# Kernel optimization log

Hardware: AMD Instinct MI355X
Metric: run time of the kernel (lower is better)

Reference implementation:

```python
import jax, jax.numpy as jnp
import numpy as np

TAU = 10.0          # tau_init
R_MAX = 8           # max(groupconvs)
GROUPCONVS = (4, 8)
PADS = (0, 8)       # (k - spat_red)//2 for k in (17, 33), spat_red = 33 - 2*8 = 17
NEG_SLOPE = 0.01    # LeakyReLU default


def lrelu(t):
    return jnp.where(t >= 0, t, NEG_SLOPE * t)


def rotate_kernel(w, theta):
    """Rotate square kernels w:[N,k,k] by theta, matching torch
    F.affine_grid + F.grid_sample (bilinear, zero padding, align_corners=False)."""
    N, k, _ = w.shape
    coords = (2.0 * jnp.arange(k) + 1.0) / k - 1.0  # normalized pixel centers
    gy, gx = jnp.meshgrid(coords, coords, indexing='ij')
    c, s = jnp.cos(theta), jnp.sin(theta)
    sx = c * gx - s * gy
    sy = s * gx + c * gy
    fx = ((sx + 1.0) * k - 1.0) / 2.0
    fy = ((sy + 1.0) * k - 1.0) / 2.0
    x0 = jnp.floor(fx).astype(jnp.int32)
    y0 = jnp.floor(fy).astype(jnp.int32)
    wf = w.reshape(N, k * k)

    def gather(yi, xi):
        valid = ((yi >= 0) & (yi < k) & (xi >= 0) & (xi < k)).astype(w.dtype)
        idx = jnp.clip(yi, 0, k - 1) * k + jnp.clip(xi, 0, k - 1)
        return wf[:, idx.reshape(-1)].reshape(N, k, k) * valid

    wx1 = fx - x0
    wy1 = fy - y0
    return (gather(y0, x0) * (1 - wy1) * (1 - wx1)
            + gather(y0, x0 + 1) * (1 - wy1) * wx1
            + gather(y0 + 1, x0) * wy1 * (1 - wx1)
            + gather(y0 + 1, x0 + 1) * wy1 * wx1)


def group_conv(x, w, b, pad):
    """GroupConv with input_rot_dim=1: x [B,1,H,W], w [O,1,1,k,k] -> [B,O,R_MAX,H',W']."""
    O, k = w.shape[0], w.shape[-1]
    w2 = w.reshape(O, k, k)
    angles = (2.0 * jnp.pi / R_MAX) * jnp.arange(R_MAX)
    tw = jax.vmap(lambda th: rotate_kernel(w2, th))(angles)   # [R,O,k,k]
    tw = jnp.transpose(tw, (1, 0, 2, 3)).reshape(O * R_MAX, 1, k, k)
    y = jax.lax.conv_general_dilated(x, tw, (1, 1), [(pad, pad), (pad, pad)],
                                     dimension_numbers=('NCHW', 'OIHW', 'NCHW'))
    B, _, H, W = y.shape
    return y.reshape(B, O, R_MAX, H, W) + b[None, :, None, None, None]


def conv1x1(h, w, b):
    # 1x1x1 Conv3d: h [B,C,R,H,W], w [O,C], b [O]
    return jnp.einsum('bcrhw,oc->borhw', h, w) + b[None, :, None, None, None]


def scatter_sum(outs, weights, axis):
    """slice_scatter-based alignment: embed smaller-rdim tensors into the
    largest one at stride max_dim//dim, weight, and sum."""
    max_out = outs[-1]
    md = max_out.shape[axis]
    total = max_out * weights[-1]
    for i, o in enumerate(outs[:-1]):
        step = md // o.shape[axis]
        idx = tuple(slice(None, None, step) if a == axis else slice(None)
                    for a in range(max_out.ndim))
        total = total + jnp.zeros_like(max_out).at[idx].set(o) * weights[i]
    return total


OFFSETS = np.array([0, np.pi / 4, np.pi / 2, 3 * np.pi / 4, np.pi,
                    -3 * np.pi / 4, -np.pi / 2, -np.pi / 4], dtype=np.float32)


def _forward(x, ksize_weight, rdim_weight, conv1_w0, conv1_b0, conv1_w1, conv1_b1,
             conv2_w, conv2_b, conva_w, conva_b, convz_w, convz_b,
             g_ksize, g_rdim, g_attn):
    # gumbel-softmax over kernel sizes (soft, tau=TAU)
    alphas = jax.nn.softmax((ksize_weight + g_ksize) / TAU)
    x_out = (alphas[0] * lrelu(group_conv(x, conv1_w0, conv1_b0, PADS[0]))
             + alphas[1] * lrelu(group_conv(x, conv1_w1, conv1_b1, PADS[1])))
    xs_out = [x_out[:, :, ::R_MAX // r] for r in GROUPCONVS]
    hs = [lrelu(conv1x1(xo, conv2_w[i], conv2_b[i])) for i, xo in enumerate(xs_out)]
    attns = [conv1x1(h, conva_w[i], conva_b[i])[:, 0] for i, h in enumerate(hs)]
    betas = jax.nn.softmax((rdim_weight + g_rdim) / TAU)
    attn = scatter_sum(attns, betas, axis=1)          # [B,R,H,W]
    offsets = jnp.asarray(OFFSETS)
    sigma = np.pi  # theta_prior; Normal(0, sigma) log-prob at offsets
    p_r = (-0.5 * (offsets / sigma) ** 2 - np.float32(np.log(sigma))
           - np.float32(0.5 * np.log(2.0 * np.pi)))[:, None, None]
    attn = attn + p_r
    B = attn.shape[0]
    flat = attn.reshape(B, -1)
    q_t_r = jax.nn.log_softmax(flat, axis=1).reshape(attn.shape)
    # F.gumbel_softmax(a, dim=-1) with default tau=1
    a_sampled = jax.nn.softmax(flat + g_attn, axis=-1).reshape(attn.shape)
    zs = [conv1x1(h, convz_w[i], convz_b[i]) for i, h in enumerate(hs)]
    z = scatter_sum(zs, betas, axis=2)                # [B,2L,R,H,W]
    # faithful to source: `thetas = [c_r(h) for c_r, h in zip(self.conv_z, hs)]`
    # reuses conv_z, so pre-refinement theta == z
    theta_pre = z
    rotation_offset = jnp.broadcast_to(offsets[None, :, None, None], a_sampled.shape)
    theta = jnp.stack((theta_pre[:, 0] + rotation_offset, theta_pre[:, 1]), axis=1)
    return attn, q_t_r, p_r, a_sampled, offsets, theta, z


def setup_inputs() -> dict:
    key = jax.random.key(0)
    ks = jax.random.split(key, 16)
    B, n, KN, L = 8, 64, 128, 2
    gum = lambda k, shape: -jnp.log(-jnp.log(
        jax.random.uniform(k, shape, jnp.float32, 1e-10, 1.0)))
    return {
        'x': jax.random.normal(ks[0], (B, 1, n, n), jnp.float32),
        'ksize_weight': 0.001 * jax.random.normal(ks[1], (2,), jnp.float32),
        'rdim_weight': 0.001 * jax.random.normal(ks[2], (2,), jnp.float32),
        'conv1_w0': 0.02 * jax.random.normal(ks[3], (KN, 1, 1, 17, 17), jnp.float32),
        'conv1_b0': 0.01 * jax.random.normal(ks[4], (KN,), jnp.float32),
        'conv1_w1': 0.02 * jax.random.normal(ks[5], (KN, 1, 1, 33, 33), jnp.float32),
        'conv1_b1': 0.01 * jax.random.normal(ks[6], (KN,), jnp.float32),
        'conv2_w': (1.0 / np.sqrt(KN)) * jax.random.normal(ks[7], (2, KN, KN), jnp.float32),
        'conv2_b': 0.01 * jax.random.normal(ks[8], (2, KN), jnp.float32),
        'conva_w': (1.0 / np.sqrt(KN)) * jax.random.normal(ks[9], (2, 1, KN), jnp.float32),
        'conva_b': 0.01 * jax.random.normal(ks[10], (2, 1), jnp.float32),
        'convz_w': (1.0 / np.sqrt(KN)) * jax.random.normal(ks[11], (2, 2 * L, KN), jnp.float32),
        'convz_b': 0.01 * jax.random.normal(ks[12], (2, 2 * L), jnp.float32),
        'g_ksize': gum(ks[13], (2,)),
        'g_rdim': gum(ks[14], (2,)),
        'g_attn': gum(ks[15], (B, R_MAX * 48 * 48)),
    }


def reference(x, ksize_weight, rdim_weight, conv1_w0, conv1_b0, conv1_w1, conv1_b1,
              conv2_w, conv2_b, conva_w, conva_b, convz_w, convz_b,
              g_ksize, g_rdim, g_attn):
    return _forward(x, ksize_weight, rdim_weight, conv1_w0, conv1_b0, conv1_w1,
                    conv1_b1, conv2_w, conv2_b, conva_w, conva_b, convz_w, convz_b,
                    g_ksize, g_rdim, g_attn)
```

## Files before the change

kernel.cpp:

```cpp
#include <hip/hip_runtime.h>
#include <hip/hip_bf16.h>
#include <math.h>

#define PI_D 3.14159265358979323846

typedef __attribute__((ext_vector_type(8))) short bf16x8;
typedef __attribute__((ext_vector_type(4))) float f32x4;
typedef __attribute__((ext_vector_type(4))) unsigned int u32x4;

#define OFF_SCAL   0u
#define OFF_W0T    4u
#define OFF_W1T    36996u
#define OFF_W2B    176388u
#define OFF_BF     192772u
#define OFF_XOUTB  1093892u
#define OFF_A0     10531076u
#define OFF_A1     10604804u
#define OFF_Z0     10752260u
#define OFF_Z1     11047172u

#define NS33 42
#define NS17 13

__device__ __forceinline__ float off_r(int r) {
  int m = (r <= 4) ? r : r - 8;
  return (float)(PI_D / 4.0) * (float)m;
}
__device__ __forceinline__ float lrelu_f(float v) { return (v >= 0.f) ? v : 0.01f * v; }
__device__ __forceinline__ short f2bf(float f) {
  __bf16 h = (__bf16)f;
  return __builtin_bit_cast(short, h);
}

__device__ __forceinline__ void unit33(int u, int& dy, int& ch) {
  if (u < 85)       { dy = (u % 17) * 2;            ch = u / 17; }
  else if (u < 165) { int v = u - 85; dy = (v & 15) * 2 + 1; ch = v >> 4; }
  else              { dy = 33; ch = 0; }
}
__device__ __forceinline__ void unit17(int u, int& dy, int& ch) {
  if (u < 27)      { dy = (u % 9) * 2;             ch = u / 9; }
  else if (u < 51) { int v = u - 27; dy = (v & 7) * 2 + 1; ch = v >> 3; }
  else             { dy = 17; ch = 0; }
}

__global__ void k_prep1(const float* __restrict__ kw, const float* __restrict__ gk,
                        const float* __restrict__ rw, const float* __restrict__ gr,
                        const float* __restrict__ w0, const float* __restrict__ w1,
                        const float* __restrict__ w2, float* __restrict__ scal,
                        float* __restrict__ w0T, float* __restrict__ w1T,
                        short* __restrict__ w2b) {
  int idx = blockIdx.x * blockDim.x + threadIdx.x;
  if (idx == 0) {
    float a0 = (kw[0] + gk[0]) * 0.1f, a1 = (kw[1] + gk[1]) * 0.1f;
    float m = fmaxf(a0, a1);
    float e0 = expf(a0 - m), e1 = expf(a1 - m), inv = 1.f / (e0 + e1);
    scal[0] = e0 * inv; scal[1] = e1 * inv;
    float b0 = (rw[0] + gr[0]) * 0.1f, b1 = (rw[1] + gr[1]) * 0.1f;
    m = fmaxf(b0, b1);
    e0 = expf(b0 - m); e1 = expf(b1 - m); inv = 1.f / (e0 + e1);
    scal[2] = e0 * inv; scal[3] = e1 * inv;
  }
  if (idx < 289 * 128) {
    int o = idx & 127, pos = idx >> 7;
    w0T[pos * 128 + o] = w0[o * 289 + pos];
    return;
  }
  idx -= 289 * 128;
  if (idx < 1089 * 128) {
    int o = idx & 127, pos = idx >> 7;
    w1T[pos * 128 + o] = w1[o * 1089 + pos];
    return;
  }
  idx -= 1089 * 128;
  if (idx < 2 * 128 * 128) w2b[idx] = f2bf(w2[idx]);
}

__global__ void k_prep2(const float* __restrict__ w0T, const float* __restrict__ w1T,
                        short* __restrict__ bfrag) {
  int t = blockIdx.x * blockDim.x + threadIdx.x;
  int o = t & 127;
  int q = t >> 7;
  int kb = q & 3; q >>= 2;
  int c = q % 55; int r = q / 55;
  float theta = (float)(PI_D / 4.0) * (float)r;
  float cth = cosf(theta), sth = sinf(theta);
  short out[8];
#pragma unroll
  for (int j = 0; j < 8; ++j) {
    float val = 0.f;
    int k, dy, ch;
    const float* wT;
    if (c < NS33) { unit33(4 * c + kb, dy, ch); k = 33; wT = w1T; }
    else          { unit17(4 * (c - NS33) + kb, dy, ch); k = 17; wT = w0T; }
    int dx = 8 * ch + j;
    if (dy < k && dx < k) {
      float cy = (2.0f * (float)dy + 1.0f) / (float)k - 1.0f;
      float cx = (2.0f * (float)dx + 1.0f) / (float)k - 1.0f;
      float sx = cth * cx - sth * cy;
      float sy = sth * cx + cth * cy;
      float fx = ((sx + 1.0f) * (float)k - 1.0f) * 0.5f;
      float fy = ((sy + 1.0f) * (float)k - 1.0f) * 0.5f;
      float x0f = floorf(fx), y0f = floorf(fy);
      int x0 = (int)x0f, y0 = (int)y0f;
      float wx1 = fx - x0f, wy1 = fy - y0f;
      float acc = 0.f;
#define CORNER(Y, X, CW) { int yy = (Y), xx = (X); \
      if (yy >= 0 && yy < k && xx >= 0 && xx < k) acc += wT[(yy * k + xx) * 128 + o] * (CW); }
      CORNER(y0,     x0,     (1.f - wy1) * (1.f - wx1));
      CORNER(y0,     x0 + 1, (1.f - wy1) * wx1);
      CORNER(y0 + 1, x0,     wy1 * (1.f - wx1));
      CORNER(y0 + 1, x0 + 1, wy1 * wx1);
#undef CORNER
      val = acc;
    }
    out[j] = f2bf(val);
  }
  *(bf16x8*)(bfrag + (size_t)t * 8) =
      (bf16x8){out[0], out[1], out[2], out[3], out[4], out[5], out[6], out[7]};
}

#define TDW 3256
#define LBOFF 1628
__global__ __launch_bounds__(256, 2) void k_conv_mfma(
    const float* __restrict__ x, const short* __restrict__ bfrag,
    const float* __restrict__ b17, const float* __restrict__ b33,
    const float* __restrict__ scal, short* __restrict__ xoutb) {
  __shared__ __align__(16) unsigned int lds[8704];
  unsigned short* lA = (unsigned short*)lds;
  unsigned short* lB = (unsigned short*)(lds + LBOFF);
  int blk = blockIdx.x;
  int r = blk & 7;
  int q = blk >> 3;
  int pt = q % 18, b = q / 18;
  int p0 = pt * 128;
  int ybase = p0 / 48;
  int tid = threadIdx.x;
  for (int idx = tid; idx < TDW; idx += 256) {
    int ty = idx / 88, tx = idx - ty * 88;
    int gy = ybase + ty - 8, gx = tx - 8;
    float v = 0.f;
    if (gy >= 0 && gy < 64 && gx >= 0 && gx < 64) v = x[(b * 64 + gy) * 64 + gx];
    unsigned short h = (unsigned short)f2bf(v);
    lA[idx] = h;
    if (idx > 0) lB[idx - 1] = h;
  }
  if (tid == 0) lB[TDW - 1] = 0;
  __syncthreads();

  int lane = tid & 63, w = tid >> 6;
  int wm = w >> 1, wn = w & 1;
  int kc = lane >> 4;
  int ln = lane & 15;
  int mloc[4];
#pragma unroll
  for (int mf = 0; mf < 4; ++mf) {
    int p = p0 + wm * 64 + (mf >> 1) * 32 + (mf & 1) + 2 * ln;
    int ym = p / 48, xm = p - ym * 48;
    mloc[mf] = (ym - ybase) * 88 + xm;
  }
  const short* bb = bfrag + (size_t)r * (55 * 4 * 128 * 8);
  int nb0 = wn * 64;

  f32x4 acc33[4][4];
#pragma unroll
  for (int mf = 0; mf < 4; ++mf)
#pragma unroll
    for (int nf = 0; nf < 4; ++nf) acc33[mf][nf] = (f32x4){0.f, 0.f, 0.f, 0.f};

#define LOADB(dst, cg)                                                          \
  {                                                                             \
    _Pragma("unroll")                                                           \
    for (int nf = 0; nf < 4; ++nf)                                              \
      dst[nf] = *(const bf16x8*)(bb + ((size_t)((cg)*4 + kc) * 128 + nb0 + nf * 16 + ln) * 8); \
  }
#define READA(dst, par, vv)                                                     \
  {                                                                             \
    int bd_ = ((vv) >> 1) + ((par) ? LBOFF : 0);                                \
    u32x4 uv_ = {lds[bd_], lds[bd_ + 1], lds[bd_ + 2], lds[bd_ + 3]};           \
    dst = __builtin_bit_cast(bf16x8, uv_);                                      \
  }

  {
    bf16x8 bc[4], bn[4];
    LOADB(bc, 0);
    for (int c = 0; c < NS33; ++c) {
      if (c + 1 < NS33) LOADB(bn, c + 1);
      int dy, ch;
      unit33(4 * c + kc, dy, ch);
      int off = dy * 88 + ch * 8;
      bf16x8 a[4];
      READA(a[0], 0, mloc[0] + off);
      READA(a[1], 1, mloc[1] + off);
      READA(a[2], 0, mloc[2] + off);
      READA(a[3], 1, mloc[3] + off);
#pragma unroll
      for (int nf = 0; nf < 4; ++nf) {
#pragma unroll
        for (int mf = 0; mf < 4; ++mf)
          acc33[mf][nf] = __builtin_amdgcn_mfma_f32_16x16x32_bf16(a[mf], bc[nf], acc33[mf][nf], 0, 0, 0);
      }
#pragma unroll
      for (int nf = 0; nf < 4; ++nf) bc[nf] = bn[nf];
    }
  }

  f32x4 acc17[4][4];
#pragma unroll
  for (int mf = 0; mf < 4; ++mf)
#pragma unroll
    for (int nf = 0; nf < 4; ++nf) acc17[mf][nf] = (f32x4){0.f, 0.f, 0.f, 0.f};
  for (int c = 0; c < NS17; ++c) {
    bf16x8 bc[4];
    LOADB(bc, NS33 + c);
    int dy, ch;
    unit17(4 * c + kc, dy, ch);
    int off = (8 + dy) * 88 + 8 + ch * 8;
    bf16x8 a[4];
    READA(a[0], 0, mloc[0] + off);
    READA(a[1], 1, mloc[1] + off);
    READA(a[2], 0, mloc[2] + off);
    READA(a[3], 1, mloc[3] + off);
#pragma unroll
    for (int nf = 0; nf < 4; ++nf) {
#pragma unroll
      for (int mf = 0; mf < 4; ++mf)
        acc17[mf][nf] = __builtin_amdgcn_mfma_f32_16x16x32_bf16(a[mf], bc[nf], acc17[mf][nf], 0, 0, 0);
    }
  }
#undef LOADB
#undef READA

  __syncthreads();
  unsigned short* sOut = (unsigned short*)lds;
  float a0s = scal[0], a1s = scal[1];
#pragma unroll
  for (int nf = 0; nf < 4; ++nf) {
    int n = nb0 + nf * 16 + ln;
    float bb17 = b17[n], bb33 = b33[n];
    int sw = n ^ (kc << 4);
#pragma unroll
    for (int mf = 0; mf < 4; ++mf) {
#pragma unroll
      for (int i = 0; i < 4; ++i) {
        int px = wm * 64 + (mf >> 1) * 32 + (mf & 1) + 8 * kc + 2 * i;
        float v = a0s * lrelu_f(acc17[mf][nf][i] + bb17)
                + a1s * lrelu_f(acc33[mf][nf][i] + bb33);
        sOut[px * 136 + sw] = (unsigned short)f2bf(v);
      }
    }
  }
  __syncthreads();
  size_t gbase = ((size_t)(b * 8 + r) * 2304 + p0) * 128;
#pragma unroll
  for (int pass = 0; pass < 8; ++pass) {
    int L16 = pass * 256 + tid;
    int px = L16 >> 4, u = L16 & 15;
    int kc3 = (px >> 3) & 3;
    int pu = u ^ (kc3 << 1);
    const unsigned int* lp = lds + px * 68 + pu * 4;
    u32x4 vv = {lp[0], lp[1], lp[2], lp[3]};
    *(u32x4*)(xoutb + gbase + (size_t)L16 * 8) = vv;
  }
}

__global__ __launch_bounds__(256, 4) void k_pw_mfma(
    const short* __restrict__ xoutb, const short* __restrict__ w2b_,
    const float* __restrict__ b2_, const float* __restrict__ wa_,
    const float* __restrict__ ba_, const float* __restrict__ wz_,
    const float* __restrict__ bz_,
    float* __restrict__ a0buf, float* __restrict__ z0buf,
    float* __restrict__ a1buf, float* __restrict__ z1buf) {
  __shared__ float sA[64];
  __shared__ float sZ[4][64];
  int blk = blockIdx.x;
  int i1 = (blk >= 1152);
  int lblk = i1 ? blk - 1152 : blk;
  int nR = i1 ? 8 : 4, rstep = i1 ? 1 : 2;
  const short* w2b = w2b_ + (i1 ? 128 * 128 : 0);
  const float* b2 = b2_ + (i1 ? 128 : 0);
  const float* wa = wa_ + (i1 ? 128 : 0);
  const float* ba = ba_ + i1;
  const float* wz = wz_ + (i1 ? 512 : 0);
  const float* bz = bz_ + (i1 ? 4 : 0);
  float* attn_out = i1 ? a1buf : a0buf;
  float* z_out = i1 ? z1buf : z0buf;

  int pblk = lblk % 36;
  int t = lblk / 36;
  int rl = t % nR;
  int b = t / nR;
  int pix0 = pblk * 64;
  int tid = threadIdx.x;
  int lane = tid & 63, w = tid >> 6;
  int kc = lane >> 4, ln = lane & 15;
  int pwave = pix0 + w * 16;
  const short* arow = xoutb + ((size_t)(b * 8 + rl * rstep) * 2304 + pwave) * 128;

  f32x4 acc[8];
#pragma unroll
  for (int nf = 0; nf < 8; ++nf) acc[nf] = (f32x4){0.f, 0.f, 0.f, 0.f};
#pragma unroll
  for (int s = 0; s < 4; ++s) {
    bf16x8 a = *(const bf16x8*)(arow + ln * 128 + s * 32 + kc * 8);
#pragma unroll
    for (int nf = 0; nf < 8; ++nf) {
      bf16x8 bv = *(const bf16x8*)(w2b + (nf * 16 + ln) * 128 + s * 32 + kc * 8);
      acc[nf] = __builtin_amdgcn_mfma_f32_16x16x32_bf16(a, bv, acc[nf], 0, 0, 0);
    }
  }

  float attn_acc[4] = {0.f, 0.f, 0.f, 0.f};
  float zacc[4][4];
#pragma unroll
  for (int j = 0; j < 4; ++j)
#pragma unroll
    for (int q = 0; q < 4; ++q) zacc[j][q] = 0.f;
#pragma unroll
  for (int nf = 0; nf < 8; ++nf) {
    int n = nf * 16 + ln;
    float bb2 = b2[n];
    float wan = wa[n];
    float wz0 = wz[n], wz1 = wz[128 + n], wz2 = wz[256 + n], wz3 = wz[384 + n];
#pragma unroll
    for (int q = 0; q < 4; ++q) {
      float h = lrelu_f(acc[nf][q] + bb2);
      attn_acc[q] = fmaf(wan, h, attn_acc[q]);
      zacc[0][q] = fmaf(wz0, h, zacc[0][q]);
      zacc[1][q] = fmaf(wz1, h, zacc[1][q]);
      zacc[2][q] = fmaf(wz2, h, zacc[2][q]);
      zacc[3][q] = fmaf(wz3, h, zacc[3][q]);
    }
  }
#pragma unroll
  for (int off = 1; off < 16; off <<= 1) {
#pragma unroll
    for (int q = 0; q < 4; ++q) {
      attn_acc[q] += __shfl_xor(attn_acc[q], off);
#pragma unroll
      for (int j = 0; j < 4; ++j) zacc[j][q] += __shfl_xor(zacc[j][q], off);
    }
  }
  if (ln == 0) {
    float ba0 = ba[0];
#pragma unroll
    for (int q = 0; q < 4; ++q) {
      int px = w * 16 + kc * 4 + q;
      sA[px] = attn_acc[q] + ba0;
#pragma unroll
      for (int j = 0; j < 4; ++j) sZ[j][px] = zacc[j][q] + bz[j];
    }
  }
  __syncthreads();
  int px = tid & 63, jj = tid >> 6;
  if (jj == 0)
    attn_out[((size_t)b * nR + rl) * 2304 + pix0 + px] = sA[px];
  z_out[(((size_t)b * 4 + jj) * nR + rl) * 2304 + pix0 + px] = sZ[jj][px];
}

__global__ void k_attn_combine(const float* __restrict__ a0buf, const float* __restrict__ a1buf,
                               const float* __restrict__ scal, float* __restrict__ out0,
                               float* __restrict__ out2, float* __restrict__ out4) {
  int idx = blockIdx.x * blockDim.x + threadIdx.x;
  if (idx < 8) {
    float off = off_r(idx);
    out4[idx] = off;
    float q = off / (float)PI_D;
    out2[idx] = -0.5f * q * q - logf((float)PI_D) - 0.5f * logf(2.0f * (float)PI_D);
  }
  if (idx >= 147456) return;
  int pix = idx % 2304;
  int t = idx / 2304;
  int r = t & 7, b = t >> 3;
  float v = scal[3] * a1buf[idx];
  if (!(r & 1)) v += scal[2] * a0buf[((size_t)b * 4 + (r >> 1)) * 2304 + pix];
  float q = off_r(r) / (float)PI_D;
  v += -0.5f * q * q - logf((float)PI_D) - 0.5f * logf(2.0f * (float)PI_D);
  out0[idx] = v;
}

__global__ __launch_bounds__(1024) void k_softmax(const float* __restrict__ out0,
                                                  const float* __restrict__ g,
                                                  float* __restrict__ out1,
                                                  float* __restrict__ out3) {
  int b = blockIdx.x;
  int tid = threadIdx.x;
  const float* v = out0 + (size_t)b * 18432;
  const float* gb = g + (size_t)b * 18432;
  float vl[18], gl[18];
  float m1 = -1e30f, m2 = -1e30f;
#pragma unroll
  for (int t = 0; t < 18; ++t) {
    float vv = v[tid + (t << 10)];
    float gg = gb[tid + (t << 10)];
    vl[t] = vv;
    gl[t] = vv + gg;
    m1 = fmaxf(m1, vv);
    m2 = fmaxf(m2, gl[t]);
  }
  __shared__ float red[32];
  for (int off = 32; off > 0; off >>= 1) {
    m1 = fmaxf(m1, __shfl_xor(m1, off));
    m2 = fmaxf(m2, __shfl_xor(m2, off));
  }
  int wid = tid >> 6, lane = tid & 63;
  if (lane == 0) { red[wid] = m1; red[wid + 16] = m2; }
  __syncthreads();
  float M1 = red[0], M2 = red[16];
#pragma unroll
  for (int w = 1; w < 16; ++w) { M1 = fmaxf(M1, red[w]); M2 = fmaxf(M2, red[w + 16]); }
  __syncthreads();
  float s1 = 0.f, s2 = 0.f;
#pragma unroll
  for (int t = 0; t < 18; ++t) { s1 += expf(vl[t] - M1); s2 += expf(gl[t] - M2); }
  for (int off = 32; off > 0; off >>= 1) {
    s1 += __shfl_xor(s1, off);
    s2 += __shfl_xor(s2, off);
  }
  if (lane == 0) { red[wid] = s1; red[wid + 16] = s2; }
  __syncthreads();
  float S1 = 0.f, S2 = 0.f;
#pragma unroll
  for (int w = 0; w < 16; ++w) { S1 += red[w]; S2 += red[w + 16]; }
  float lse = M1 + logf(S1);
  float inv2 = 1.0f / S2;
  float* o1 = out1 + (size_t)b * 18432;
  float* o3 = out3 + (size_t)b * 18432;
#pragma unroll
  for (int t = 0; t < 18; ++t) {
    o1[tid + (t << 10)] = vl[t] - lse;
    o3[tid + (t << 10)] = expf(gl[t] - M2) * inv2;
  }
}

__global__ void k_ztheta(const float* __restrict__ z0buf, const float* __restrict__ z1buf,
                         const float* __restrict__ scal, float* __restrict__ out5,
                         float* __restrict__ out6) {
  int idx = blockIdx.x * blockDim.x + threadIdx.x;
  if (idx >= 589824) return;
  int pix = idx % 2304;
  int t = idx / 2304;
  int r = t & 7;
  t >>= 3;
  int c = t & 3;
  int b = t >> 2;
  float v = scal[3] * z1buf[idx];
  if (!(r & 1)) v += scal[2] * z0buf[(((size_t)b * 4 + c) * 4 + (r >> 1)) * 2304 + pix];
  out6[idx] = v;
  if (c == 0)      out5[(((size_t)b * 2 + 0) * 8 + r) * 2304 + pix] = v + off_r(r);
  else if (c == 1) out5[(((size_t)b * 2 + 1) * 8 + r) * 2304 + pix] = v;
}

extern "C" void kernel_launch(void* const* d_in, const int* in_sizes, int n_in,
                              void* d_out, int out_size, void* d_ws, size_t ws_size,
                              hipStream_t stream) {
  const float* x   = (const float*)d_in[0];
  const float* ksz = (const float*)d_in[1];
  const float* rdw = (const float*)d_in[2];
  const float* w0  = (const float*)d_in[3];
  const float* b0  = (const float*)d_in[4];
  const float* w1  = (const float*)d_in[5];
  const float* b1  = (const float*)d_in[6];
  const float* w2  = (const float*)d_in[7];
  const float* b2  = (const float*)d_in[8];
  const float* wa  = (const float*)d_in[9];
  const float* ba  = (const float*)d_in[10];
  const float* wz  = (const float*)d_in[11];
  const float* bz  = (const float*)d_in[12];
  const float* gks = (const float*)d_in[13];
  const float* grd = (const float*)d_in[14];
  const float* gat = (const float*)d_in[15];
  float* out = (float*)d_out;
  float* ws  = (float*)d_ws;

  float* scal = ws + OFF_SCAL;
  float* w0T  = ws + OFF_W0T;
  float* w1T  = ws + OFF_W1T;
  short* w2b  = (short*)(ws + OFF_W2B);
  short* bfr  = (short*)(ws + OFF_BF);
  short* xoutb = (short*)(ws + OFF_XOUTB);
  float* a0b  = ws + OFF_A0;
  float* a1b  = ws + OFF_A1;
  float* z0b  = ws + OFF_Z0;
  float* z1b  = ws + OFF_Z1;

  float* out0 = out;
  float* out1 = out + 147456;
  float* out2 = out + 294912;
  float* out3 = out + 294920;
  float* out4 = out + 442376;
  float* out5 = out + 442384;
  float* out6 = out + 737296;

  k_prep1<<<817, 256, 0, stream>>>(ksz, gks, rdw, grd, w0, w1, w2, scal, w0T, w1T, w2b);
  k_prep2<<<880, 256, 0, stream>>>(w0T, w1T, bfr);
  k_conv_mfma<<<1152, 256, 0, stream>>>(x, bfr, b0, b1, scal, xoutb);
  k_pw_mfma<<<3456, 256, 0, stream>>>(xoutb, w2b, b2, wa, ba, wz, bz,
                                      a0b, z0b, a1b, z1b);
  k_attn_combine<<<576, 256, 0, stream>>>(a0b, a1b, scal, out0, out2, out4);
  k_softmax<<<8, 1024, 0, stream>>>(out0, gat, out1, out3);
  k_ztheta<<<2304, 256, 0, stream>>>(z0b, z1b, scal, out5, out6);
}
```

Baseline: 256.8 us.

## Store eight shifted input copies in LDS for aligned 128-bit A-fragment reads

The conv kernel now keeps eight copies of the bf16 input tile in LDS, each shifted by one element, in place of two. The pixel-to-row mapping is changed so every A-fragment load is a single aligned 16-byte LDS read instead of four scalar dword reads. The output swizzle is updated to match the new pixel mapping, and launch bounds are raised to request three blocks per CU. The cost is more LDS per block (about 52KB) and eight stores per input element during tile setup, and occupancy may be limited by LDS rather than registers.

```diff
diff --git a/kernel.cpp b/kernel.cpp
--- a/kernel.cpp
+++ b/kernel.cpp
@@ -120,14 +120,13 @@
 }
 
 #define TDW 3256
-#define LBOFF 1628
-__global__ __launch_bounds__(256, 2) void k_conv_mfma(
+#define CPYD 1632
+__global__ __launch_bounds__(256, 3) void k_conv_mfma(
     const float* __restrict__ x, const short* __restrict__ bfrag,
     const float* __restrict__ b17, const float* __restrict__ b33,
     const float* __restrict__ scal, short* __restrict__ xoutb) {
-  __shared__ __align__(16) unsigned int lds[8704];
-  unsigned short* lA = (unsigned short*)lds;
-  unsigned short* lB = (unsigned short*)(lds + LBOFF);
+  __shared__ __align__(16) unsigned int lds[8 * CPYD];
+  unsigned short* ls = (unsigned short*)lds;
   int blk = blockIdx.x;
   int r = blk & 7;
   int q = blk >> 3;
@@ -141,22 +140,26 @@
     float v = 0.f;
     if (gy >= 0 && gy < 64 && gx >= 0 && gx < 64) v = x[(b * 64 + gy) * 64 + gx];
     unsigned short h = (unsigned short)f2bf(v);
-    lA[idx] = h;
-    if (idx > 0) lB[idx - 1] = h;
-  }
-  if (tid == 0) lB[TDW - 1] = 0;
+#pragma unroll
+    for (int g = 0; g < 8; ++g) {
+      int pos = idx - g;
+      if (pos >= 0) ls[g * 3264 + pos] = h;
+    }
+  }
   __syncthreads();
 
   int lane = tid & 63, w = tid >> 6;
   int wm = w >> 1, wn = w & 1;
   int kc = lane >> 4;
   int ln = lane & 15;
-  int mloc[4];
+  int baseD[4];
 #pragma unroll
   for (int mf = 0; mf < 4; ++mf) {
-    int p = p0 + wm * 64 + (mf >> 1) * 32 + (mf & 1) + 2 * ln;
+    int g = 4 * wm + mf;
+    int p = p0 + g + 8 * ln;
     int ym = p / 48, xm = p - ym * 48;
-    mloc[mf] = (ym - ybase) * 88 + xm;
+    int ts = (ym - ybase) * 88 + xm;
+    baseD[mf] = g * CPYD + ((ts - g) >> 1);
   }
   const short* bb = bfrag + (size_t)r * (55 * 4 * 128 * 8);
   int nb0 = wn * 64;
@@ -173,12 +176,8 @@
     for (int nf = 0; nf < 4; ++nf)                                              \
       dst[nf] = *(const bf16x8*)(bb + ((size_t)((cg)*4 + kc) * 128 + nb0 + nf * 16 + ln) * 8); \
   }
-#define READA(dst, par, vv)                                                     \
-  {                                                                             \
-    int bd_ = ((vv) >> 1) + ((par) ? LBOFF : 0);                                \
-    u32x4 uv_ = {lds[bd_], lds[bd_ + 1], lds[bd_ + 2], lds[bd_ + 3]};           \
-    dst = __builtin_bit_cast(bf16x8, uv_);                                      \
-  }
+#define READA(dst, mf, offD)                                                    \
+  dst = __builtin_bit_cast(bf16x8, *(const u32x4*)(lds + baseD[mf] + (offD)));
 
   {
     bf16x8 bc[4], bn[4];
@@ -187,12 +186,12 @@
       if (c + 1 < NS33) LOADB(bn, c + 1);
       int dy, ch;
       unit33(4 * c + kc, dy, ch);
-      int off = dy * 88 + ch * 8;
+      int offD = dy * 44 + ch * 4;
       bf16x8 a[4];
-      READA(a[0], 0, mloc[0] + off);
-      READA(a[1], 1, mloc[1] + off);
-      READA(a[2], 0, mloc[2] + off);
-      READA(a[3], 1, mloc[3] + off);
+      READA(a[0], 0, offD);
+      READA(a[1], 1, offD);
+      READA(a[2], 2, offD);
+      READA(a[3], 3, offD);
 #pragma unroll
       for (int nf = 0; nf < 4; ++nf) {
 #pragma unroll
@@ -214,12 +213,12 @@
     LOADB(bc, NS33 + c);
     int dy, ch;
     unit17(4 * c + kc, dy, ch);
-    int off = (8 + dy) * 88 + 8 + ch * 8;
+    int offD = (8 + dy) * 44 + 4 + ch * 4;
     bf16x8 a[4];
-    READA(a[0], 0, mloc[0] + off);
-    READA(a[1], 1, mloc[1] + off);
-    READA(a[2], 0, mloc[2] + off);
-    READA(a[3], 1, mloc[3] + off);
+    READA(a[0], 0, offD);
+    READA(a[1], 1, offD);
+    READA(a[2], 2, offD);
+    READA(a[3], 3, offD);
 #pragma unroll
     for (int nf = 0; nf < 4; ++nf) {
 #pragma unroll
@@ -233,16 +232,18 @@
   __syncthreads();
   unsigned short* sOut = (unsigned short*)lds;
   float a0s = scal[0], a1s = scal[1];
+  int dq = lane >> 4;
 #pragma unroll
   for (int nf = 0; nf < 4; ++nf) {
     int n = nb0 + nf * 16 + ln;
     float bb17 = b17[n], bb33 = b33[n];
-    int sw = n ^ (kc << 4);
+    int sw = n ^ (dq << 4);
 #pragma unroll
     for (int mf = 0; mf < 4; ++mf) {
+      int g = 4 * wm + mf;
 #pragma unroll
       for (int i = 0; i < 4; ++i) {
-        int px = wm * 64 + (mf >> 1) * 32 + (mf & 1) + 8 * kc + 2 * i;
+        int px = g + 32 * dq + 8 * i;
         float v = a0s * lrelu_f(acc17[mf][nf][i] + bb17)
                 + a1s * lrelu_f(acc33[mf][nf][i] + bb33);
         sOut[px * 136 + sw] = (unsigned short)f2bf(v);
@@ -255,8 +256,8 @@
   for (int pass = 0; pass < 8; ++pass) {
     int L16 = pass * 256 + tid;
     int px = L16 >> 4, u = L16 & 15;
-    int kc3 = (px >> 3) & 3;
-    int pu = u ^ (kc3 << 1);
+    int dq3 = (px >> 5) & 3;
+    int pu = u ^ (dq3 << 1);
     const unsigned int* lp = lds + px * 68 + pu * 4;
     u32x4 vv = {lp[0], lp[1], lp[2], lp[3]};
     *(u32x4*)(xoutb + gbase + (size_t)L16 * 8) = vv;
```

New measurement: 268.3 us. 4.5% more time.
